# Kernel tuning notes

Measured on AMD Instinct MI355X. Metric: run time of the kernel, lower is better.

## Reference

```python
import jax, jax.numpy as jnp
import numpy as np


def _make_stencil():
    # Fixed perception filters from the source: identity, Sobel-x, Sobel-y, Laplacian.
    ident = np.array([[0, 0, 0], [0, 1, 0], [0, 0, 0]], np.float32)
    sobel_x = np.array([[-1, 0, 1], [-2, 0, 2], [-1, 0, 1]], np.float32)
    sobel_y = sobel_x.T
    lap = np.array([[1, 2, 1], [2, -12, 2], [1, 2, 1]], np.float32)
    # HWIO with I=1 -> depthwise (feature_group_count=4): channel i filtered by filter i.
    return jnp.asarray(np.stack([ident, sobel_x, sobel_y, lap], axis=-1)[:, :, None, :])


def setup_inputs() -> dict:
    key = jax.random.key(0)
    k1, k2, k3 = jax.random.split(key, 3)
    B, S, C, H = 32, 512, 4, 6
    x = jax.random.uniform(k1, (B, S, S, C), jnp.float32)  # grid state in [0,1)
    w1_kernel = jax.random.normal(k2, (C, H), jnp.float32) * 0.3  # 1x1 conv 4->6
    w1_bias = jnp.zeros((H,), jnp.float32)
    w2_kernel = jax.random.normal(k3, (H, C), jnp.float32) * 0.3  # 1x1 conv 6->4, no bias
    # update_rate=1 -> floor(uniform+1) == 1 everywhere (deterministic all-ones mask)
    update_mask = jnp.ones((B, S, S, 1), jnp.float32)
    stencil = _make_stencil()
    return {"x": x, "w1_kernel": w1_kernel, "w1_bias": w1_bias,
            "w2_kernel": w2_kernel, "stencil": stencil, "update_mask": update_mask}


def reference(x, w1_kernel, w1_bias, w2_kernel, stencil, update_mask):
    # Circular pad by 1 in H and W (the Cropping2D/Concatenate dance in the source).
    xp = jnp.pad(x, ((0, 0), (1, 1), (1, 1), (0, 0)), mode="wrap")
    # Depthwise 3x3 perception conv (grouped tf.nn.conv2d with I=1, 4 groups).
    perc = jax.lax.conv_general_dilated(
        xp, stencil, window_strides=(1, 1), padding="VALID",
        dimension_numbers=("NHWC", "HWIO", "NHWC"), feature_group_count=4)
    # Two pointwise convs (1x1): relu then sigmoid.
    h = jax.nn.relu(jnp.einsum("bhwc,cf->bhwf", perc, w1_kernel) + w1_bias)
    y = jax.nn.sigmoid(jnp.einsum("bhwf,fc->bhwc", h, w2_kernel))
    # Stochastic cell update blend (mask is all ones for update_rate=1).
    return x * (1.0 - update_mask) + y * update_mask
```

## Files before the change

kernel.cpp:

```cpp
#include <hip/hip_runtime.h>


#define S_DIM 512
#define ROWS 8
#define B_DIM 32

typedef float f32x4 __attribute__((ext_vector_type(4)));
typedef float f32x2 __attribute__((ext_vector_type(2)));

__global__ __launch_bounds__(256) void nca_step_kernel(
    const float4* __restrict__ x,
    const float*  __restrict__ w1,
    const float*  __restrict__ b1,
    const float*  __restrict__ w2,
    f32x4*        __restrict__ out)
{
    const int w  = blockIdx.x * 256 + threadIdx.x;
    const int h0 = blockIdx.y * ROWS;
    const int b  = blockIdx.z;

    const int wm = (w - 1) & (S_DIM - 1);
    const int wp = (w + 1) & (S_DIM - 1);

    const size_t img_off = (size_t)b * (S_DIM * S_DIM);
    const float4* __restrict__ img = x + img_off;

    float4 cL[ROWS + 2], cC[ROWS + 2], cR[ROWS + 2];
#pragma unroll
    for (int r = 0; r < ROWS + 2; ++r) {
        const int rr = (h0 + r - 1) & (S_DIM - 1);
        const int rb = rr * S_DIM;
        cL[r] = img[rb + wm];
        cC[r] = img[rb + w ];
        cR[r] = img[rb + wp];
    }

#pragma unroll
    for (int k = 0; k < ROWS; k += 2) {
        f32x2 P0, P1, P2, P3, Cx, Cy, Cz, Cw;
#pragma unroll
        for (int t = 0; t < 2; ++t) {
            const float4 Lt = cL[k + t],     Ct = cC[k + t],     Rt = cR[k + t];
            const float4 Lm = cL[k + t + 1], Cm = cC[k + t + 1], Rm = cR[k + t + 1];
            const float4 Lb = cL[k + t + 2], Cb = cC[k + t + 2], Rb = cR[k + t + 2];

            P0[t] = Cm.x;
            P1[t] = (Rt.y - Lt.y) + 2.f * (Rm.y - Lm.y) + (Rb.y - Lb.y);
            P2[t] = (Lb.z - Lt.z) + 2.f * (Cb.z - Ct.z) + (Rb.z - Rt.z);
            P3[t] = Lt.w + 2.f * Ct.w + Rt.w
                  + 2.f * Lm.w - 12.f * Cm.w + 2.f * Rm.w
                  + Lb.w + 2.f * Cb.w + Rb.w;
        }

        f32x2 hb[6];
#pragma unroll
        for (int j = 0; j < 6; ++j) {
            f32x2 v = (f32x2)(b1[j]);
            v = __builtin_elementwise_fma(P0, (f32x2)(w1[0 * 6 + j]), v);
            v = __builtin_elementwise_fma(P1, (f32x2)(w1[1 * 6 + j]), v);
            v = __builtin_elementwise_fma(P2, (f32x2)(w1[2 * 6 + j]), v);
            v = __builtin_elementwise_fma(P3, (f32x2)(w1[3 * 6 + j]), v);
            hb[j] = __builtin_elementwise_max(v, (f32x2)(0.f));
        }

        f32x2 acc[4];
#pragma unroll
        for (int c = 0; c < 4; ++c) {
            f32x2 v = (f32x2)(0.f);
#pragma unroll
            for (int j = 0; j < 6; ++j)
                v = __builtin_elementwise_fma(hb[j], (f32x2)(w2[j * 4 + c]), v);
            acc[c] = v;
        }

#pragma unroll
        for (int t = 0; t < 2; ++t) {
            f32x4 o;
#pragma unroll
            for (int c = 0; c < 4; ++c)
                o[c] = __builtin_amdgcn_rcpf(1.f + __expf(-acc[c][t]));
            __builtin_nontemporal_store(
                o, &out[img_off + (size_t)(h0 + k + t) * S_DIM + w]);
        }
    }
}

extern "C" void kernel_launch(void* const* d_in, const int* in_sizes, int n_in,
                              void* d_out, int out_size, void* d_ws, size_t ws_size,
                              hipStream_t stream) {
    const float4* x  = (const float4*)d_in[0];
    const float*  w1 = (const float*)d_in[1];
    const float*  b1 = (const float*)d_in[2];
    const float*  w2 = (const float*)d_in[3];
    f32x4* out = (f32x4*)d_out;

    dim3 grid(S_DIM / 256, S_DIM / ROWS, B_DIM);
    nca_step_kernel<<<grid, 256, 0, stream>>>(x, w1, b1, w2, out);
}
```

Measured before the change: 49.99 us.

## Stage input tile with halo in shared memory instead of per-thread neighbor loads

Each block now loads a (TR+2)x(TC+2) float4 tile, including the wrapped left/right halo columns, into LDS and reads its 3x3 neighbourhoods from there. This replaces the three redundant global loads per row (left, centre, right) that each thread issued before. Rows per block drop from 8 to 4, which raises the vertical halo overhead and adds a __syncthreads and LDS traffic in exchange for fewer global/L2 requests.

```diff
diff --git a/kernel.cpp b/kernel.cpp
--- a/kernel.cpp
+++ b/kernel.cpp
@@ -2,8 +2,8 @@
 
 
 #define S_DIM 512
-#define ROWS 8
-#define B_DIM 32
+#define TR 4
+#define TC 256
 
 typedef float f32x4 __attribute__((ext_vector_type(4)));
 typedef float f32x2 __attribute__((ext_vector_type(2)));
@@ -15,34 +15,45 @@
     const float*  __restrict__ w2,
     f32x4*        __restrict__ out)
 {
-    const int w  = blockIdx.x * 256 + threadIdx.x;
-    const int h0 = blockIdx.y * ROWS;
-    const int b  = blockIdx.z;
+    __shared__ float4 tile[TR + 2][TC + 2];
 
-    const int wm = (w - 1) & (S_DIM - 1);
-    const int wp = (w + 1) & (S_DIM - 1);
+    const int tid = threadIdx.x;
+    const int w0  = blockIdx.x * TC;
+    const int h0  = blockIdx.y * TR;
+    const int b   = blockIdx.z;
 
     const size_t img_off = (size_t)b * (S_DIM * S_DIM);
     const float4* __restrict__ img = x + img_off;
 
-    float4 cL[ROWS + 2], cC[ROWS + 2], cR[ROWS + 2];
 #pragma unroll
-    for (int r = 0; r < ROWS + 2; ++r) {
-        const int rr = (h0 + r - 1) & (S_DIM - 1);
-        const int rb = rr * S_DIM;
-        cL[r] = img[rb + wm];
-        cC[r] = img[rb + w ];
-        cR[r] = img[rb + wp];
+    for (int r = 0; r < TR + 2; ++r) {
+        const int gr = (h0 + r - 1) & (S_DIM - 1);
+        tile[r][tid + 1] = img[gr * S_DIM + w0 + tid];
     }
+    if (tid < 2 * (TR + 2)) {
+        const int r    = tid >> 1;
+        const int side = tid & 1;
+        const int gr   = (h0 + r - 1) & (S_DIM - 1);
+        const int gc   = side ? ((w0 + TC) & (S_DIM - 1)) : ((w0 - 1) & (S_DIM - 1));
+        tile[r][side ? TC + 1 : 0] = img[gr * S_DIM + gc];
+    }
+    __syncthreads();
 
 #pragma unroll
-    for (int k = 0; k < ROWS; k += 2) {
-        f32x2 P0, P1, P2, P3, Cx, Cy, Cz, Cw;
+    for (int k = 0; k < TR; k += 2) {
+        float4 Wn[4][3];
+#pragma unroll
+        for (int r = 0; r < 4; ++r)
+#pragma unroll
+            for (int c = 0; c < 3; ++c)
+                Wn[r][c] = tile[k + r][tid + c];
+
+        f32x2 P0, P1, P2, P3;
 #pragma unroll
         for (int t = 0; t < 2; ++t) {
-            const float4 Lt = cL[k + t],     Ct = cC[k + t],     Rt = cR[k + t];
-            const float4 Lm = cL[k + t + 1], Cm = cC[k + t + 1], Rm = cR[k + t + 1];
-            const float4 Lb = cL[k + t + 2], Cb = cC[k + t + 2], Rb = cR[k + t + 2];
+            const float4 Lt = Wn[t][0],     Ct = Wn[t][1],     Rt = Wn[t][2];
+            const float4 Lm = Wn[t + 1][0], Cm = Wn[t + 1][1], Rm = Wn[t + 1][2];
+            const float4 Lb = Wn[t + 2][0], Cb = Wn[t + 2][1], Rb = Wn[t + 2][2];
 
             P0[t] = Cm.x;
             P1[t] = (Rt.y - Lt.y) + 2.f * (Rm.y - Lm.y) + (Rb.y - Lb.y);
@@ -80,7 +91,7 @@
             for (int c = 0; c < 4; ++c)
                 o[c] = __builtin_amdgcn_rcpf(1.f + __expf(-acc[c][t]));
             __builtin_nontemporal_store(
-                o, &out[img_off + (size_t)(h0 + k + t) * S_DIM + w]);
+                o, &out[img_off + (size_t)(h0 + k + t) * S_DIM + w0 + tid]);
         }
     }
 }
@@ -94,6 +105,6 @@
     const float*  w2 = (const float*)d_in[3];
     f32x4* out = (f32x4*)d_out;
 
-    dim3 grid(S_DIM / 256, S_DIM / ROWS, B_DIM);
-    nca_step_kernel<<<grid, 256, 0, stream>>>(x, w1, b1, w2, out);
+    dim3 grid(S_DIM / TC, S_DIM / TR, 32);
+    nca_step_kernel<<<grid, TC, 0, stream>>>(x, w1, b1, w2, out);
 }
```

Result: slower. 57.61 us (+15.2%).

## Share horizontal stencil neighbors via wavefront shuffles instead of triple loads

Applied to the files above, without the earlier changes.

Each thread now loads only its own column and computes vertical partial sums for the Sobel and Laplacian filters. Left and right neighbor values come from cross-lane shuffles, and the edge lanes of each 64-wide wavefront issue extra loads for the halo column. This cuts global load instructions roughly threefold, and the stencil arithmetic is factored into separable vertical-then-horizontal sums. In exchange it adds six shuffles per row and a divergent branch taken by the edge lanes.

```diff
diff --git a/kernel.cpp b/kernel.cpp
--- a/kernel.cpp
+++ b/kernel.cpp
@@ -3,7 +3,6 @@
 
 #define S_DIM 512
 #define ROWS 8
-#define B_DIM 32
 
 typedef float f32x4 __attribute__((ext_vector_type(4)));
 typedef float f32x2 __attribute__((ext_vector_type(2)));
@@ -15,41 +14,65 @@
     const float*  __restrict__ w2,
     f32x4*        __restrict__ out)
 {
-    const int w  = blockIdx.x * 256 + threadIdx.x;
-    const int h0 = blockIdx.y * ROWS;
-    const int b  = blockIdx.z;
-
-    const int wm = (w - 1) & (S_DIM - 1);
-    const int wp = (w + 1) & (S_DIM - 1);
+    const int tid  = threadIdx.x;
+    const int lane = tid & 63;
+    const int w    = blockIdx.x * 256 + tid;
+    const int h0   = blockIdx.y * ROWS;
+    const int b    = blockIdx.z;
 
     const size_t img_off = (size_t)b * (S_DIM * S_DIM);
     const float4* __restrict__ img = x + img_off;
 
-    float4 cL[ROWS + 2], cC[ROWS + 2], cR[ROWS + 2];
+    float4 c[ROWS + 2];
 #pragma unroll
     for (int r = 0; r < ROWS + 2; ++r) {
         const int rr = (h0 + r - 1) & (S_DIM - 1);
-        const int rb = rr * S_DIM;
-        cL[r] = img[rb + wm];
-        cC[r] = img[rb + w ];
-        cR[r] = img[rb + wp];
+        c[r] = img[rr * S_DIM + w];
     }
+
+    float evy[ROWS], evz[ROWS], evw[ROWS];
+#pragma unroll
+    for (int k = 0; k < ROWS; ++k) { evy[k] = 0.f; evz[k] = 0.f; evw[k] = 0.f; }
+    const bool isL = (lane == 0), isR = (lane == 63);
+    if (isL || isR) {
+        const int ew = (isL ? (w - 1) : (w + 1)) & (S_DIM - 1);
+        float4 ec[ROWS + 2];
+#pragma unroll
+        for (int r = 0; r < ROWS + 2; ++r) {
+            const int rr = (h0 + r - 1) & (S_DIM - 1);
+            ec[r] = img[rr * S_DIM + ew];
+        }
+#pragma unroll
+        for (int k = 0; k < ROWS; ++k) {
+            evy[k] = ec[k].y + 2.f * ec[k + 1].y + ec[k + 2].y;
+            evz[k] = ec[k + 2].z - ec[k].z;
+            evw[k] = ec[k].w + 2.f * ec[k + 1].w + ec[k + 2].w;
+        }
+    }
+
+    const int lm = (lane + 63) & 63;
+    const int lp = (lane + 1) & 63;
 
 #pragma unroll
     for (int k = 0; k < ROWS; k += 2) {
-        f32x2 P0, P1, P2, P3, Cx, Cy, Cz, Cw;
+        f32x2 P0, P1, P2, P3;
 #pragma unroll
         for (int t = 0; t < 2; ++t) {
-            const float4 Lt = cL[k + t],     Ct = cC[k + t],     Rt = cR[k + t];
-            const float4 Lm = cL[k + t + 1], Cm = cC[k + t + 1], Rm = cR[k + t + 1];
-            const float4 Lb = cL[k + t + 2], Cb = cC[k + t + 2], Rb = cR[k + t + 2];
+            const int kk = k + t;
+            const float vy = c[kk].y + 2.f * c[kk + 1].y + c[kk + 2].y;
+            const float vz = c[kk + 2].z - c[kk].z;
+            const float vw = c[kk].w + 2.f * c[kk + 1].w + c[kk + 2].w;
 
-            P0[t] = Cm.x;
-            P1[t] = (Rt.y - Lt.y) + 2.f * (Rm.y - Lm.y) + (Rb.y - Lb.y);
-            P2[t] = (Lb.z - Lt.z) + 2.f * (Cb.z - Ct.z) + (Rb.z - Rt.z);
-            P3[t] = Lt.w + 2.f * Ct.w + Rt.w
-                  + 2.f * Lm.w - 12.f * Cm.w + 2.f * Rm.w
-                  + Lb.w + 2.f * Cb.w + Rb.w;
+            float vyL = __shfl(vy, lm, 64), vyR = __shfl(vy, lp, 64);
+            float vzL = __shfl(vz, lm, 64), vzR = __shfl(vz, lp, 64);
+            float vwL = __shfl(vw, lm, 64), vwR = __shfl(vw, lp, 64);
+            if (isL) { vyL = evy[kk]; vzL = evz[kk]; vwL = evw[kk]; }
+            if (isR) { vyR = evy[kk]; vzR = evz[kk]; vwR = evw[kk]; }
+
+            P0[t] = c[kk + 1].x;
+            P1[t] = vyR - vyL;
+            P2[t] = vzL + 2.f * vz + vzR;
+            P3[t] = vwL + 2.f * vw + vwR - 16.f * c[kk + 1].w;
         }
 
         f32x2 hb[6];
@@ -65,20 +88,20 @@
 
         f32x2 acc[4];
 #pragma unroll
-        for (int c = 0; c < 4; ++c) {
+        for (int c2 = 0; c2 < 4; ++c2) {
             f32x2 v = (f32x2)(0.f);
 #pragma unroll
             for (int j = 0; j < 6; ++j)
-                v = __builtin_elementwise_fma(hb[j], (f32x2)(w2[j * 4 + c]), v);
-            acc[c] = v;
+                v = __builtin_elementwise_fma(hb[j], (f32x2)(w2[j * 4 + c2]), v);
+            acc[c2] = v;
         }
 
 #pragma unroll
         for (int t = 0; t < 2; ++t) {
             f32x4 o;
 #pragma unroll
-            for (int c = 0; c < 4; ++c)
-                o[c] = __builtin_amdgcn_rcpf(1.f + __expf(-acc[c][t]));
+            for (int c2 = 0; c2 < 4; ++c2)
+                o[c2] = __builtin_amdgcn_rcpf(1.f + __expf(-acc[c2][t]));
             __builtin_nontemporal_store(
                 o, &out[img_off + (size_t)(h0 + k + t) * S_DIM + w]);
         }
@@ -94,6 +117,6 @@
     const float*  w2 = (const float*)d_in[3];
     f32x4* out = (f32x4*)d_out;
 
-    dim3 grid(S_DIM / 256, S_DIM / ROWS, B_DIM);
+    dim3 grid(S_DIM / 256, S_DIM / ROWS, 32);
     nca_step_kernel<<<grid, 256, 0, stream>>>(x, w1, b1, w2, out);
 }
```

Result: slower. 53.00 us (+6.0%).
